# Optimization experiments

Measured on AMD Instinct MI355X. Metric: run time of the kernel, lower is better.

## Reference

```python
import jax, jax.numpy as jnp
import numpy as np

WS = 7        # kernel_size
DIL = 1       # dilation
HEADS = 8


def _reflect(idx, L):
    # stnls-style reflect bounds (no edge duplication): -1 -> 1, L -> L-2
    period = 2 * (L - 1)
    m = jnp.mod(idx, period)
    return jnp.where(m > L - 1, period - m, m)


def setup_inputs() -> dict:
    key = jax.random.key(0)
    k1, k2, k3 = jax.random.split(key, 3)
    T, H, W, C = 8, 64, 64, 256
    x = jax.random.normal(k1, (T, H, W, C), jnp.float32)
    # flows: (1, T, 2*wt, 2, H, W) with wt=1; channel 0 = di (rows), 1 = dj (cols)
    flows = jax.random.normal(k2, (1, T, 2, 2, H, W), jnp.float32) * 2.0
    W_qk = jax.random.normal(k3, (2 * C, C), jnp.float32) * 0.02
    return {"x": x, "flows": flows, "W_qk": W_qk}


def _slot(q, k, tp, fli, flj):
    # q,k: (HD,T,H,W,hd); tp: (T,) frame index per query frame; fli,flj: (T,H,W) flow
    HD, T, H, W, hd = q.shape
    di = jnp.round(fli).astype(jnp.int32)   # itype='int': integer flow offsets
    dj = jnp.round(flj).astype(jnp.int32)
    ci = jnp.arange(H, dtype=jnp.int32)[None, :, None] + di   # (T,H,W) window centers
    cj = jnp.arange(W, dtype=jnp.int32)[None, None, :] + dj
    kg = k[:, tp]                                             # (HD,T,H,W,hd) keys of searched frame
    off = DIL * (jnp.arange(WS, dtype=jnp.int32) - WS // 2)
    t_idx = jnp.arange(T)[:, None, None, None]
    ii = jnp.arange(H, dtype=jnp.int32)[None, :, None]
    jj = jnp.arange(W, dtype=jnp.int32)[None, None, :, None]
    dt = (tp - jnp.arange(T)).astype(jnp.int32)               # (T,)
    scores, offs = [], []
    for a in range(WS):  # structural loop over window rows to bound intermediates
        li = _reflect(ci + off[a], H)                                    # (T,H,W)
        lj = _reflect(cj[..., None] + off[None, None, None, :], W)       # (T,H,W,WS)
        kn = kg[:, t_idx, li[..., None], lj, :]                          # (HD,T,H,W,WS,hd)
        scores.append(jnp.einsum('dthwf,dthwbf->dthwb', q, kn))         # (HD,T,H,W,WS)
        o = jnp.stack([
            jnp.broadcast_to(dt[:, None, None, None], (T, H, W, WS)),
            jnp.broadcast_to((li - ii[:, :, :]) [..., None], (T, H, W, WS)),
            lj - jj], axis=-1)                                           # (T,H,W,WS,3)
        offs.append(o)
    s = jnp.stack(scores, axis=4).reshape(HD, T, H, W, WS * WS)
    o = jnp.stack(offs, axis=3).reshape(T, H, W, WS * WS, 3)
    return s, o


def reference(x, flows, W_qk):
    T, H, W, C = x.shape
    hd = C // HEADS
    scale = hd ** (-0.5)
    qk = (x @ W_qk.T).reshape(T, H, W, 2, HEADS, hd)
    q = jnp.transpose(qk[:, :, :, 0], (3, 0, 1, 2, 4))  # (HD,T,H,W,hd)
    k = jnp.transpose(qk[:, :, :, 1], (3, 0, 1, 2, 4))
    t = jnp.arange(T)
    tp1 = jnp.where(t + 1 < T, t + 1, t - 2)   # forward frame, window shifted at boundary
    tp2 = jnp.where(t - 1 >= 0, t - 1, t + 2)  # backward frame
    z = jnp.zeros((T, H, W), x.dtype)
    s0, o0 = _slot(q, k, t, z, z)
    s1, o1 = _slot(q, k, tp1, flows[0, :, 0, 0], flows[0, :, 0, 1])
    s2, o2 = _slot(q, k, tp2, flows[0, :, 1, 0], flows[0, :, 1, 1])
    attn = scale * jnp.concatenate([s0, s1, s2], axis=-1)[None]   # (1,HD,T,H,W,K)
    fk = jnp.concatenate([o0, o1, o2], axis=3)                    # (T,H,W,K,3)
    flows_k = jnp.broadcast_to(fk[None, None], (1, HEADS) + fk.shape)
    return attn, flows_k
```

## Files before the change

kernel.cpp:

```cpp
#include <hip/hip_runtime.h>
#include <hip/hip_bf16.h>

#define TT_    8
#define HEADS_ 8
#define NB_    147
#define NPIX   32768
#define NTASK  (NPIX*NB_)
#define ROWS_  (NPIX + 512)

typedef _Float16 half8 __attribute__((ext_vector_type(8)));
typedef _Float16 h2    __attribute__((ext_vector_type(2)));
typedef float    f32x4 __attribute__((ext_vector_type(4)));

__device__ __forceinline__ int reflect64(int v) {
  int m = v % 126;
  m += (m >> 31) & 126;
  return (m > 63) ? (126 - m) : m;
}

__device__ __forceinline__ float dot2f(h2 a, h2 b, float c) {
#if __has_builtin(__builtin_amdgcn_fdot2)
  return __builtin_amdgcn_fdot2(a, b, c, false);
#else
  return c + (float)a[0]*(float)b[0] + (float)a[1]*(float)b[1];
#endif
}

__device__ __forceinline__ float dpp_xor1(float x) {
  int r = __builtin_amdgcn_mov_dpp(__builtin_bit_cast(int, x), 0xB1, 0xF, 0xF, true);
  return __builtin_bit_cast(float, r);
}
__device__ __forceinline__ float dpp_xor2(float x) {
  int r = __builtin_amdgcn_mov_dpp(__builtin_bit_cast(int, x), 0x4E, 0xF, 0xF, true);
  return __builtin_bit_cast(float, r);
}

__global__ __launch_bounds__(256) void prepack(
    const float* __restrict__ x, const float* __restrict__ wqk,
    _Float16* __restrict__ outp) {
  int o  = (int)blockIdx.x * 256 + (int)threadIdx.x;
  int r  = o & 15, quad = (o >> 4) & 3, ks = (o >> 6) & 7, mt = o >> 9;
  int row = mt * 16 + r;
  const float* src = (row < NPIX) ? (x + (size_t)row * 256)
                                  : (wqk + (size_t)(row - NPIX) * 256);
  int col = (ks * 4 + quad) * 8;
  float4 a = *(const float4*)(src + col);
  float4 b = *(const float4*)(src + col + 4);
  half8 h;
  h[0]=(_Float16)a.x; h[1]=(_Float16)a.y; h[2]=(_Float16)a.z; h[3]=(_Float16)a.w;
  h[4]=(_Float16)b.x; h[5]=(_Float16)b.y; h[6]=(_Float16)b.z; h[7]=(_Float16)b.w;
  ((half8*)outp)[o] = h;
}

__global__ __launch_bounds__(256) void qk_gemm(
    const _Float16* __restrict__ Ap,
    _Float16* __restrict__ qws, _Float16* __restrict__ kws) {
  const half8* A8 = (const half8*)Ap;
  const half8* B8 = (const half8*)(Ap + (size_t)NPIX * 256);
  int bid  = (int)blockIdx.x;
  int mblk = bid >> 2, nblk = bid & 3;
  int lane = (int)threadIdx.x & 63, wv = (int)threadIdx.x >> 6;
  int wm = mblk * 128 + (wv >> 1) * 64;
  int wn = nblk * 128 + (wv & 1) * 64;
  int r = lane & 15, quad = lane >> 4;

  f32x4 acc[4][4] = {};
#pragma unroll
  for (int ks = 0; ks < 8; ks++) {
    half8 af[4], bf[4];
#pragma unroll
    for (int im = 0; im < 4; im++)
      af[im] = A8[((((wm >> 4) + im) * 8 + ks) * 4 + quad) * 16 + r];
#pragma unroll
    for (int in = 0; in < 4; in++)
      bf[in] = B8[((((wn >> 4) + in) * 8 + ks) * 4 + quad) * 16 + r];
#pragma unroll
    for (int im = 0; im < 4; im++)
#pragma unroll
      for (int in = 0; in < 4; in++)
        acc[im][in] = __builtin_amdgcn_mfma_f32_16x16x32_f16(
            af[im], bf[in], acc[im][in], 0, 0, 0);
  }

  _Float16* dst = (wn < 256) ? qws : kws;
  int nsub = (wn < 256) ? 0 : 256;
#pragma unroll
  for (int im = 0; im < 4; im++)
#pragma unroll
    for (int in = 0; in < 4; in++) {
      int n = wn + in * 16 + r - nsub;
#pragma unroll
      for (int reg = 0; reg < 4; reg++) {
        int m = wm + im * 16 + quad * 4 + reg;
        dst[(size_t)m * 256 + n] = (_Float16)acc[im][in][reg];
      }
    }
}

__global__ __launch_bounds__(256) void attn_kernel(
    const float* __restrict__ flows,
    const _Float16* __restrict__ qws, const _Float16* __restrict__ kws,
    float* __restrict__ out) {
  __shared__ int      s_info[256];
  __shared__ __attribute__((aligned(16))) _Float16 s_q[3 * 32 * 8];
  __shared__ __attribute__((aligned(16))) float    s_attn[8 * 260];
  __shared__ __attribute__((aligned(16))) float    s_flow[768];

  int nbq = (int)gridDim.x >> 3;
  int blk = ((int)blockIdx.x & 7) * nbq + ((int)blockIdx.x >> 3);
  int tx  = (int)threadIdx.x;
  int btid0 = blk * 256;
  int p0 = (int)((unsigned)btid0 / 147u);

  half8 vq = {};
  int qslot = -1;
  if (tx < 96) {
    int pix = tx >> 5, s = tx & 31;
    int p = p0 + pix; if (p > NPIX - 1) p = NPIX - 1;
    vq = *(const half8*)(qws + (size_t)p * 256 + s * 8);
    qslot = pix * 32 + s;
  }

  {
    int tid = btid0 + tx;
    unsigned p = (unsigned)tid / 147u;
    int nb = tid - (int)(p * 147u);
    int t = (int)(p >> 12), hw = (int)(p & 4095u);
    int h = hw >> 6, w = hw & 63;
    int slot = nb / 49;
    int rr = nb - slot * 49;
    int a = rr / 7, b = rr - a * 7;
    int tp = t, di = 0, dj = 0;
    if (slot > 0) {
      int si = slot - 1;
      di = (int)rintf(flows[(size_t)((t * 2 + si) * 2 + 0) * 4096 + hw]);
      dj = (int)rintf(flows[(size_t)((t * 2 + si) * 2 + 1) * 4096 + hw]);
      tp = (slot == 1) ? ((t + 1 < TT_) ? t + 1 : t - 2)
                       : ((t - 1 >= 0)  ? t - 1 : t + 2);
    }
    int li = reflect64(h + di + a - 3);
    int lj = reflect64(w + dj + b - 3);
    int kidx = (tp << 12) + (li << 6) + lj;
    int pixloc = (int)p - p0;
    s_info[tx] = kidx | (pixloc << 20);
    s_flow[tx * 3 + 0] = (float)(tp - t);
    s_flow[tx * 3 + 1] = (float)(li - h);
    s_flow[tx * 3 + 2] = (float)(lj - w);
  }
  if (qslot >= 0) ((half8*)s_q)[qslot] = vq;
  __syncthreads();

  int lane = tx & 63, wv = tx >> 6;
  int j = lane & 7, g = lane >> 3;
  const float scale = 0.17677669529663687f;
#pragma unroll
  for (int it = 0; it < 8; it++) {
    int tb = wv * 64 + it * 8 + g;
    int info = s_info[tb];
    int kidx = info & 0xFFFFF;
    int pixloc = info >> 20;
    const half8* kp = (const half8*)(kws + ((size_t)kidx << 8)) + j;
    const half8* qp = ((const half8*)s_q) + pixloc * 32 + j;
    float acc[4];
#pragma unroll
    for (int c = 0; c < 4; c++) {
      half8 k8 = kp[c * 8];
      half8 q8 = qp[c * 8];
      float s = 0.f;
#pragma unroll
      for (int u = 0; u < 8; u += 2) {
        h2 ka = { k8[u], k8[u + 1] };
        h2 qa = { q8[u], q8[u + 1] };
        s = dot2f(ka, qa, s);
      }
      acc[c] = s;
    }
#pragma unroll
    for (int c = 0; c < 4; c++) {
      float t = acc[c];
      t += dpp_xor1(t);
      t += dpp_xor2(t);
      if ((lane & 3) == 0)
        s_attn[(2 * c + ((lane >> 2) & 1)) * 260 + tb] = t * scale;
    }
  }
  __syncthreads();

  const f32x4* sa4 = (const f32x4*)s_attn;
#pragma unroll
  for (int o = 0; o < 2; o++) {
    int gg = tx + o * 256;
    int hh = gg >> 6, idx = gg & 63;
    f32x4 v = sa4[hh * 65 + idx];
    __builtin_nontemporal_store(v, (f32x4*)(out + (size_t)hh * NTASK + btid0) + idx);
  }
  float* fo = out + (size_t)HEADS_ * NTASK;
  const f32x4* sf4 = (const f32x4*)s_flow;
#pragma unroll
  for (int o = 0; o < 6; o++) {
    int gg = tx + o * 256;
    int hh = gg / 192, idx = gg - hh * 192;
    f32x4 v = sf4[idx];
    __builtin_nontemporal_store(v, (f32x4*)(fo + (size_t)hh * NTASK * 3 + (size_t)btid0 * 3) + idx);
  }
}

extern "C" void kernel_launch(void* const* d_in, const int* in_sizes, int n_in,
                              void* d_out, int out_size, void* d_ws, size_t ws_size,
                              hipStream_t stream) {
  const float* x     = (const float*)d_in[0];
  const float* flows = (const float*)d_in[1];
  const float* wqk   = (const float*)d_in[2];
  float* out = (float*)d_out;

  _Float16* qws = (_Float16*)d_ws;
  _Float16* kws = qws + (size_t)NPIX * 256;
  _Float16* Ap  = kws + (size_t)NPIX * 256;

  prepack<<<dim3(ROWS_ * 32 / 256), dim3(256), 0, stream>>>(x, wqk, Ap);
  qk_gemm<<<dim3(1024), dim3(256), 0, stream>>>(Ap, qws, kws);
  attn_kernel<<<dim3(NTASK / 256), dim3(256), 0, stream>>>(flows, qws, kws, out);
}
```

Baseline: 660.7 us.

## Make attention kernel wave-local, replacing block barriers with wave barriers and shuffles

Restructures the attention kernel so each wavefront owns its 64 tasks end to end, with its own q, score and flow staging in shared memory. Block-wide __syncthreads are replaced by an LDS waitcnt plus a wave barrier, and the per-task index info is broadcast with __shfl instead of a shared array. The aim is to remove block synchronisation stalls and let waves progress independently, with launch bounds raised to request higher occupancy. In exchange, each wave loads its own q rows (64 loads per wave instead of 96 per block), which adds redundant q traffic.

Measured after the change: 678.1 us. 1.03x slower.

```diff
diff --git a/kernel.cpp b/kernel.cpp
--- a/kernel.cpp
+++ b/kernel.cpp
@@ -97,32 +97,32 @@
     }
 }
 
-__global__ __launch_bounds__(256) void attn_kernel(
+__global__ __launch_bounds__(256, 4) void attn_kernel(
     const float* __restrict__ flows,
     const _Float16* __restrict__ qws, const _Float16* __restrict__ kws,
     float* __restrict__ out) {
-  __shared__ int      s_info[256];
-  __shared__ __attribute__((aligned(16))) _Float16 s_q[3 * 32 * 8];
-  __shared__ __attribute__((aligned(16))) float    s_attn[8 * 260];
-  __shared__ __attribute__((aligned(16))) float    s_flow[768];
+  __shared__ __attribute__((aligned(16))) _Float16 s_q[4 * 64 * 8];
+  __shared__ __attribute__((aligned(16))) float    s_attn[4 * 8 * 64];
+  __shared__ __attribute__((aligned(16))) float    s_flow[4 * 192];
 
   int nbq = (int)gridDim.x >> 3;
   int blk = ((int)blockIdx.x & 7) * nbq + ((int)blockIdx.x >> 3);
   int tx  = (int)threadIdx.x;
+  int lane = tx & 63, wv = tx >> 6;
   int btid0 = blk * 256;
-  int p0 = (int)((unsigned)btid0 / 147u);
-
-  half8 vq = {};
-  int qslot = -1;
-  if (tx < 96) {
-    int pix = tx >> 5, s = tx & 31;
-    int p = p0 + pix; if (p > NPIX - 1) p = NPIX - 1;
-    vq = *(const half8*)(qws + (size_t)p * 256 + s * 8);
-    qslot = pix * 32 + s;
-  }
+  int wtid0 = btid0 + wv * 64;
+  int pw0 = (int)((unsigned)wtid0 / 147u);
 
   {
-    int tid = btid0 + tx;
+    int pix = lane >> 5, s = lane & 31;
+    int p = pw0 + pix; if (p > NPIX - 1) p = NPIX - 1;
+    half8 vq = *(const half8*)(qws + (size_t)p * 256 + s * 8);
+    ((half8*)s_q)[wv * 64 + lane] = vq;
+  }
+
+  int myinfo;
+  {
+    int tid = wtid0 + lane;
     unsigned p = (unsigned)tid / 147u;
     int nb = tid - (int)(p * 147u);
     int t = (int)(p >> 12), hw = (int)(p & 4095u);
@@ -141,26 +141,24 @@
     int li = reflect64(h + di + a - 3);
     int lj = reflect64(w + dj + b - 3);
     int kidx = (tp << 12) + (li << 6) + lj;
-    int pixloc = (int)p - p0;
-    s_info[tx] = kidx | (pixloc << 20);
-    s_flow[tx * 3 + 0] = (float)(tp - t);
-    s_flow[tx * 3 + 1] = (float)(li - h);
-    s_flow[tx * 3 + 2] = (float)(lj - w);
-  }
-  if (qslot >= 0) ((half8*)s_q)[qslot] = vq;
-  __syncthreads();
-
-  int lane = tx & 63, wv = tx >> 6;
+    int pixloc = (int)p - pw0;
+    myinfo = kidx | (pixloc << 20);
+    s_flow[wv * 192 + lane * 3 + 0] = (float)(tp - t);
+    s_flow[wv * 192 + lane * 3 + 1] = (float)(li - h);
+    s_flow[wv * 192 + lane * 3 + 2] = (float)(lj - w);
+  }
+  asm volatile("s_waitcnt lgkmcnt(0)" ::: "memory");
+  __builtin_amdgcn_wave_barrier();
+
   int j = lane & 7, g = lane >> 3;
   const float scale = 0.17677669529663687f;
 #pragma unroll
   for (int it = 0; it < 8; it++) {
-    int tb = wv * 64 + it * 8 + g;
-    int info = s_info[tb];
+    int info = __shfl(myinfo, it * 8 + g, 64);
     int kidx = info & 0xFFFFF;
     int pixloc = info >> 20;
     const half8* kp = (const half8*)(kws + ((size_t)kidx << 8)) + j;
-    const half8* qp = ((const half8*)s_q) + pixloc * 32 + j;
+    const half8* qp = ((const half8*)s_q) + wv * 64 + pixloc * 32 + j;
     float acc[4];
 #pragma unroll
     for (int c = 0; c < 4; c++) {
@@ -181,27 +179,28 @@
       t += dpp_xor1(t);
       t += dpp_xor2(t);
       if ((lane & 3) == 0)
-        s_attn[(2 * c + ((lane >> 2) & 1)) * 260 + tb] = t * scale;
-    }
-  }
-  __syncthreads();
-
-  const f32x4* sa4 = (const f32x4*)s_attn;
+        s_attn[wv * 512 + (2 * c + ((lane >> 2) & 1)) * 64 + it * 8 + g] = t * scale;
+    }
+  }
+  asm volatile("s_waitcnt lgkmcnt(0)" ::: "memory");
+  __builtin_amdgcn_wave_barrier();
+
 #pragma unroll
   for (int o = 0; o < 2; o++) {
-    int gg = tx + o * 256;
-    int hh = gg >> 6, idx = gg & 63;
-    f32x4 v = sa4[hh * 65 + idx];
-    __builtin_nontemporal_store(v, (f32x4*)(out + (size_t)hh * NTASK + btid0) + idx);
+    int u = o * 64 + lane;
+    int hh = u >> 4, idx = u & 15;
+    f32x4 v = *(const f32x4*)(s_attn + wv * 512 + hh * 64 + idx * 4);
+    __builtin_nontemporal_store(v,
+        (f32x4*)(out + (size_t)hh * NTASK + wtid0) + idx);
   }
   float* fo = out + (size_t)HEADS_ * NTASK;
-  const f32x4* sf4 = (const f32x4*)s_flow;
-#pragma unroll
-  for (int o = 0; o < 6; o++) {
-    int gg = tx + o * 256;
-    int hh = gg / 192, idx = gg - hh * 192;
-    f32x4 v = sf4[idx];
-    __builtin_nontemporal_store(v, (f32x4*)(fo + (size_t)hh * NTASK * 3 + (size_t)btid0 * 3) + idx);
+#pragma unroll
+  for (int rep = 0; rep < 6; rep++) {
+    int u = rep * 64 + lane;
+    int hh = u / 48, idx = u - hh * 48;
+    f32x4 v = *(const f32x4*)(s_flow + wv * 192 + idx * 4);
+    __builtin_nontemporal_store(v,
+        (f32x4*)(fo + (size_t)hh * NTASK * 3 + (size_t)wtid0 * 3) + idx);
   }
 }
 
```
